# Kernel tuning notes

Measured on AMD Instinct MI355X. Metric: run time of the kernel, lower is better.

## Reference

```python
import jax, jax.numpy as jnp
import numpy as np

B, C, H, W = 64, 1280, 16, 16
S = H * W  # 256 spatial positions


def setup_inputs() -> dict:
    key = jax.random.key(0)
    kx, kk, kq, kv, kr, ka = jax.random.split(key, 6)
    x = jax.random.normal(kx, (B, C, H, W), dtype=jnp.float32)
    scale = 0.02
    Wk = jax.random.normal(kk, (C, C), dtype=jnp.float32) * scale
    Wq = jax.random.normal(kq, (C, C), dtype=jnp.float32) * scale
    Wv = jax.random.normal(kv, (C, C), dtype=jnp.float32) * scale
    Wr = jax.random.normal(kr, (C, C), dtype=jnp.float32) * scale
    # nn.Parameter(torch.zeros(1)) in the original; init nonzero so the
    # attention branch actually contributes.
    alpha = jax.random.normal(ka, (1,), dtype=jnp.float32) * 0.1
    return {"x": x, "Wk": Wk, "Wq": Wq, "Wv": Wv, "Wr": Wr, "alpha": alpha}


def reference(x, Wk, Wq, Wv, Wr, alpha):
    b, c = x.shape[0], x.shape[1]
    s = x.shape[2] * x.shape[3]
    xf = x.reshape(b, c, s)  # [B, C, S]
    # 1x1 convs == per-position channel matmuls
    K = jnp.einsum("oc,bcs->bos", Wk, xf)  # [B, C, S]
    Q = jnp.einsum("oc,bcs->bos", Wq, xf)
    V = jnp.einsum("oc,bcs->bos", Wv, xf)
    # scores[b,i,j] = sum_c K[b,c,i] * Q[b,c,j]
    scores = jnp.einsum("bci,bcj->bij", K, Q) / (c ** 0.5)  # [B, S, S]
    # torch.nn.Softmax2d on a 3D tensor applies softmax over dim=-3,
    # i.e. across the BATCH axis here (faithful to the original code).
    A = jax.nn.softmax(scores, axis=0)
    # attended[b,c,i] = sum_j A[b,i,j] * V[b,c,j]
    att = jnp.einsum("bij,bcj->bci", A, V)  # [B, C, S]
    refined = jnp.einsum("oc,bcs->bos", Wr, att).reshape(x.shape)
    out = alpha * refined + x  # use_alpha=True, skip connection
    return out
```

## Files before the change

kernel.cpp:

```cpp
#include <hip/hip_runtime.h>
#include <hip/hip_bf16.h>
#include <cstdint>
#include <cmath>

#define B_ 64
#define C_ 1280
#define S_ 256

typedef __attribute__((ext_vector_type(8))) short short8;
typedef __attribute__((ext_vector_type(4))) float f32x4;

typedef const __attribute__((address_space(1))) char gch;
typedef __attribute__((address_space(3))) char lch;

__device__ __forceinline__ void gload_lds16(const void* g, void* l) {
    __builtin_amdgcn_global_load_lds((gch*)g, (lch*)l, 16, 0, 0);
}

__device__ __forceinline__ unsigned short f2bu(float f) {
    __hip_bfloat16 h = __float2bfloat16(f);
    return *reinterpret_cast<unsigned short*>(&h);
}

__global__ void cvt_weights(const float* __restrict__ Wk, const float* __restrict__ Wq,
                            const float* __restrict__ Wv, const float* __restrict__ Wr,
                            __hip_bfloat16* __restrict__ Wcat, __hip_bfloat16* __restrict__ Wrb) {
    const int nW = C_ * C_;
    int i = blockIdx.x * blockDim.x + threadIdx.x;
    if (i >= 4 * nW) return;
    int seg = i / nW, off = i - seg * nW;
    float v;
    if (seg == 0) v = Wk[off];
    else if (seg == 1) v = Wq[off];
    else if (seg == 2) v = Wv[off];
    else v = Wr[off];
    if (seg < 3) Wcat[i] = __float2bfloat16(v);
    else Wrb[off] = __float2bfloat16(v);
}

__global__ void transpose_cvt(const float* __restrict__ x, __hip_bfloat16* __restrict__ xT) {
    __shared__ float tile[32][33];
    int b = blockIdx.z;
    int s0 = blockIdx.x * 32, c0 = blockIdx.y * 32;
    int tx = threadIdx.x, ty = threadIdx.y;
    const float* xb = x + (long)b * C_ * S_;
#pragma unroll
    for (int dy = 0; dy < 32; dy += 8)
        tile[ty + dy][tx] = xb[(long)(c0 + ty + dy) * S_ + s0 + tx];
    __syncthreads();
    __hip_bfloat16* xTb = xT + (long)b * S_ * C_;
#pragma unroll
    for (int dy = 0; dy < 32; dy += 8)
        xTb[(long)(s0 + ty + dy) * C_ + c0 + tx] = __float2bfloat16(tile[tx][ty + dy]);
}

__global__ void softmax_b(const float* __restrict__ scores, __hip_bfloat16* __restrict__ Abf) {
    int tid = blockIdx.x * blockDim.x + threadIdx.x;
    float r[64];
    float mx = -1e30f;
#pragma unroll
    for (int b = 0; b < 64; ++b) {
        r[b] = scores[(long)b * 65536 + tid];
        mx = fmaxf(mx, r[b]);
    }
    float sum = 0.f;
#pragma unroll
    for (int b = 0; b < 64; ++b) {
        r[b] = __expf(r[b] - mx);
        sum += r[b];
    }
    float inv = 1.0f / sum;
#pragma unroll
    for (int b = 0; b < 64; ++b)
        Abf[(long)b * 65536 + tid] = __float2bfloat16(r[b] * inv);
}


#define PH_TOP()                                                \
    do {                                                        \
        __builtin_amdgcn_sched_barrier(0);                      \
        __builtin_amdgcn_s_barrier();                           \
        asm volatile("s_waitcnt lgkmcnt(0)" ::: "memory");      \
        __builtin_amdgcn_sched_barrier(0);                      \
        __builtin_amdgcn_s_setprio(1);                          \
    } while (0)

#define PH_BOT()                                                \
    do {                                                        \
        __builtin_amdgcn_s_setprio(0);                          \
        __builtin_amdgcn_sched_barrier(0);                      \
        __builtin_amdgcn_s_barrier();                           \
    } while (0)

#define PH_BOT_WAIT(LAST_)                                          \
    do {                                                            \
        __builtin_amdgcn_s_setprio(0);                              \
        __builtin_amdgcn_sched_barrier(0);                          \
        if (LAST_) asm volatile("s_waitcnt vmcnt(0)" ::: "memory"); \
        else       asm volatile("s_waitcnt vmcnt(2)" ::: "memory"); \
        __builtin_amdgcn_s_barrier();                               \
    } while (0)

#define MFMA_Q(MO, NO, BFV)                                                                        \
    _Pragma("unroll") for (int m = 0; m < 4; ++m) {                                                \
        _Pragma("unroll") for (int n = 0; n < 2; ++n) {                                            \
            acc[m + MO][n + NO] = __builtin_amdgcn_mfma_f32_16x16x32_bf16(                         \
                af[m][0], BFV[n][0], acc[m + MO][n + NO], 0, 0, 0);                                \
            acc[m + MO][n + NO] = __builtin_amdgcn_mfma_f32_16x16x32_bf16(                         \
                af[m][1], BFV[n][1], acc[m + MO][n + NO], 0, 0, 0);                                \
        }                                                                                          \
    }

#define LOAD_A(SLOT, RO)                                  \
    _Pragma("unroll") for (int m = 0; m < 4; ++m) {       \
        af[m][0] = RD(SLOT, (RO) + m * 16 + l15, 0);      \
        af[m][1] = RD(SLOT, (RO) + m * 16 + l15, 1);      \
    }

#define LOAD_B(SLOT, BFV, NO)                                    \
    _Pragma("unroll") for (int n = 0; n < 2; ++n) {              \
        BFV[n][0] = RD(SLOT, rB0 + ((NO) + n) * 16 + l15, 0);    \
        BFV[n][1] = RD(SLOT, rB0 + ((NO) + n) * 16 + l15, 1);    \
    }

template <int MODE>
__global__ __launch_bounds__(512, 2) void gemm8p(
    const __hip_bfloat16* __restrict__ A, const __hip_bfloat16* __restrict__ Bm,
    __hip_bfloat16* __restrict__ Cc, int lda, int ldb, int ldc,
    int Kd, int tilesN, int nwg, int vTile,
    __hip_bfloat16* __restrict__ Vb,
    const float* __restrict__ xF, const float* __restrict__ alphaPtr,
    float* __restrict__ outF) {
    __shared__ char lds[131072];

    int bid = blockIdx.x;
    int cpx = nwg >> 3;
    int swz = (bid & 7) * cpx + (bid >> 3);
    int tm = swz / tilesN, tn = swz - tm * tilesN;

    int t = threadIdx.x;
    int lane = t & 63, w = t >> 6;
    int wm = w >> 2, wn = w & 3;
    int l15 = lane & 15, lhi = lane >> 4;
    int rB0 = (wn & 1) * 64;
    const int sA0 = wm, sB0 = 2 + (wn >> 1);
    const int sA1 = 4 + wm, sB1 = 6 + (wn >> 1);

    const __hip_bfloat16* aT = A + (long)tm * 256 * lda;
    const __hip_bfloat16* bT = Bm + (long)tn * 256 * ldb;

    int srow = t >> 3;
    int sc = ((t & 7) ^ (srow & 7)) * 8;
    const __hip_bfloat16* stA = aT + (long)srow * lda + sc;
    const __hip_bfloat16* stB = bT + (long)srow * ldb + sc;

    auto STAGE = [&](int kt, int j) {
        const __hip_bfloat16* p;
        long ldg;
        if (j < 2) { p = stA + (long)j * 128 * lda + kt * 64; ldg = lda; }
        else       { p = stB + (long)(j - 2) * 128 * ldb + kt * 64; ldg = ldb; }
        char* slot = lds + (((kt & 1) * 4 + j) << 14);
        gload_lds16(p, slot + t * 16);
        gload_lds16(p + 64 * ldg, slot + t * 16 + 8192);
    };

    auto RD = [&](int slotIdx, int row, int kk) -> short8 {
        const char* p = lds + (slotIdx << 14) + row * 128 +
                        ((((kk << 2) + lhi) ^ (row & 7)) << 4);
        return *reinterpret_cast<const short8*>(p);
    };

    f32x4 acc[8][4];
#pragma unroll
    for (int i = 0; i < 8; ++i)
#pragma unroll
        for (int j = 0; j < 4; ++j) acc[i][j] = (f32x4){0.f, 0.f, 0.f, 0.f};

    short8 af[4][2], b0v[2][2], b1v[2][2];

    STAGE(0, 0); STAGE(0, 1); STAGE(0, 2); STAGE(0, 3); STAGE(1, 0);
    asm volatile("s_waitcnt vmcnt(2)" ::: "memory");
    __builtin_amdgcn_s_barrier();
    __builtin_amdgcn_sched_barrier(0);

    const int NTH = Kd >> 7;
    for (int i = 0; i < NTH; ++i) {
        const bool last = (i == NTH - 1);
        const int kt0 = 2 * i, kt1 = 2 * i + 1;

        LOAD_A(sA0, 0)
        LOAD_B(sB0, b0v, 0)
        STAGE(kt1, 1);
        PH_TOP();
        MFMA_Q(0, 0, b0v)
        PH_BOT();

        LOAD_B(sB0, b1v, 2)
        STAGE(kt1, 2);
        PH_TOP();
        MFMA_Q(0, 2, b1v)
        PH_BOT();

        LOAD_A(sA0, 64)
        STAGE(kt1, 3);
        PH_TOP();
        MFMA_Q(4, 2, b1v)
        PH_BOT();

        if (!last) STAGE(kt0 + 2, 0);
        PH_TOP();
        MFMA_Q(4, 0, b0v)
        PH_BOT_WAIT(last);

        LOAD_A(sA1, 0)
        LOAD_B(sB1, b0v, 0)
        if (!last) STAGE(kt0 + 2, 1);
        PH_TOP();
        MFMA_Q(0, 0, b0v)
        PH_BOT();

        LOAD_B(sB1, b1v, 2)
        if (!last) STAGE(kt0 + 2, 2);
        PH_TOP();
        MFMA_Q(0, 2, b1v)
        PH_BOT();

        LOAD_A(sA1, 64)
        if (!last) STAGE(kt0 + 2, 3);
        PH_TOP();
        MFMA_Q(4, 2, b1v)
        PH_BOT();

        if (!last) STAGE(kt0 + 3, 0);
        PH_TOP();
        MFMA_Q(4, 0, b0v)
        __builtin_amdgcn_s_setprio(0);
        __builtin_amdgcn_sched_barrier(0);
        if (!last) asm volatile("s_waitcnt vmcnt(2)" ::: "memory");
        __builtin_amdgcn_s_barrier();
    }

    if constexpr (MODE == 1) {
        if (tn < vTile) {
            long crow0 = (long)tm * 256 + wm * 128;
            int cc0 = tn * 256 + wn * 64;
#pragma unroll
            for (int m = 0; m < 8; ++m) {
                long gm = crow0 + m * 16 + lhi * 4;
#pragma unroll
                for (int n = 0; n < 4; ++n) {
                    int gn = cc0 + n * 16 + l15;
#pragma unroll
                    for (int r = 0; r < 4; ++r)
                        Cc[(gm + r) * ldc + gn] = __float2bfloat16(acc[m][n][r]);
                }
            }
        } else {
            unsigned short* Vus = (unsigned short*)Vb;
            int cb0 = (tn - vTile) * 256 + wn * 64;
#pragma unroll
            for (int m = 0; m < 8; ++m) {
                int s0 = wm * 128 + m * 16 + lhi * 4;
#pragma unroll
                for (int n = 0; n < 4; ++n) {
                    int c = cb0 + n * 16 + l15;
                    ushort4 pk;
                    pk.x = f2bu(acc[m][n][0]);
                    pk.y = f2bu(acc[m][n][1]);
                    pk.z = f2bu(acc[m][n][2]);
                    pk.w = f2bu(acc[m][n][3]);
                    *reinterpret_cast<ushort4*>(&Vus[((long)(tm * 1280 + c) << 8) + s0]) = pk;
                }
            }
        }
    } else {
        float alpha = alphaPtr[0];
#pragma unroll
        for (int m = 0; m < 8; ++m) {
            int s0 = wm * 128 + m * 16 + lhi * 4;
#pragma unroll
            for (int n = 0; n < 4; ++n) {
                int c = tn * 256 + wn * 64 + n * 16 + l15;
                long base = ((long)(tm * 1280 + c) << 8) + s0;
                f32x4 xv = *reinterpret_cast<const f32x4*>(xF + base);
                f32x4 o;
#pragma unroll
                for (int r = 0; r < 4; ++r) o[r] = alpha * acc[m][n][r] + xv[r];
                *reinterpret_cast<f32x4*>(outF + base) = o;
            }
        }
    }
}

template <int MODE>
__global__ __launch_bounds__(256) void gemm_tn(
    const __hip_bfloat16* __restrict__ A, long aBatch, int lda,
    const __hip_bfloat16* __restrict__ Bm, long bBatch, int ldb,
    void* __restrict__ Cp, long cBatch, int ldc,
    int Kd, int tilesM, int tilesN, float scale) {
    __shared__ __hip_bfloat16 lA[128 * 32];
    __shared__ __hip_bfloat16 lB[128 * 32];

    int tiles = tilesM * tilesN;
    int blk = blockIdx.x;
    int b = blk / tiles;
    int rem = blk - b * tiles;
    int tm = rem / tilesN;
    int tn = rem - tm * tilesN;

    int t = threadIdx.x;
    int lane = t & 63;
    int w = t >> 6;
    int wm = w >> 1, wn = w & 1;
    int lane15 = lane & 15, lhi = lane >> 4;

    const __hip_bfloat16* Ab = A + (long)b * aBatch + (long)tm * 128 * lda;
    const __hip_bfloat16* Bb = Bm + (long)b * bBatch + (long)tn * 128 * ldb;

    f32x4 acc[4][4];
#pragma unroll
    for (int i = 0; i < 4; ++i)
#pragma unroll
        for (int j = 0; j < 4; ++j) acc[i][j] = (f32x4){0.f, 0.f, 0.f, 0.f};

    int e0 = t * 8;
    int r0 = e0 >> 5;
    int c0e = e0 & 31;

    for (int k0 = 0; k0 < Kd; k0 += 32) {
        gload_lds16(Ab + (long)r0 * lda + k0 + c0e, lA + e0);
        gload_lds16(Ab + (long)(r0 + 64) * lda + k0 + c0e, lA + 2048 + e0);
        gload_lds16(Bb + (long)r0 * ldb + k0 + c0e, lB + e0);
        gload_lds16(Bb + (long)(r0 + 64) * ldb + k0 + c0e, lB + 2048 + e0);
        __syncthreads();

        short8 af[4], bf[4];
#pragma unroll
        for (int i = 0; i < 4; ++i)
            af[i] = *reinterpret_cast<const short8*>(lA + (wm * 64 + i * 16 + lane15) * 32 + lhi * 8);
#pragma unroll
        for (int j = 0; j < 4; ++j)
            bf[j] = *reinterpret_cast<const short8*>(lB + (wn * 64 + j * 16 + lane15) * 32 + lhi * 8);
#pragma unroll
        for (int i = 0; i < 4; ++i)
#pragma unroll
            for (int j = 0; j < 4; ++j)
                acc[i][j] = __builtin_amdgcn_mfma_f32_16x16x32_bf16(af[i], bf[j], acc[i][j], 0, 0, 0);
        __syncthreads();
    }

    long cOff = (long)b * cBatch;
    if (MODE == 0) {
        __hip_bfloat16* Cb = (__hip_bfloat16*)Cp + cOff;
#pragma unroll
        for (int i = 0; i < 4; ++i) {
            int gm = tm * 128 + wm * 64 + i * 16 + lhi * 4;
#pragma unroll
            for (int j = 0; j < 4; ++j) {
                int gn = tn * 128 + wn * 64 + j * 16 + lane15;
#pragma unroll
                for (int r = 0; r < 4; ++r)
                    Cb[(long)(gm + r) * ldc + gn] = __float2bfloat16(acc[i][j][r]);
            }
        }
    } else {
        float* Cb = (float*)Cp + cOff;
#pragma unroll
        for (int i = 0; i < 4; ++i) {
            int gm = tm * 128 + wm * 64 + i * 16 + lhi * 4;
#pragma unroll
            for (int j = 0; j < 4; ++j) {
                int gn = tn * 128 + wn * 64 + j * 16 + lane15;
#pragma unroll
                for (int r = 0; r < 4; ++r)
                    Cb[(long)(gm + r) * ldc + gn] = acc[i][j][r] * scale;
            }
        }
    }
}

extern "C" void kernel_launch(void* const* d_in, const int* in_sizes, int n_in,
                              void* d_out, int out_size, void* d_ws, size_t ws_size,
                              hipStream_t stream) {
    const float* x = (const float*)d_in[0];
    const float* Wk = (const float*)d_in[1];
    const float* Wq = (const float*)d_in[2];
    const float* Wv = (const float*)d_in[3];
    const float* Wr = (const float*)d_in[4];
    const float* alphaPtr = (const float*)d_in[5];

    char* ws = (char*)d_ws;
    size_t off = 0;
    auto alloc = [&](size_t bytes) {
        char* p = ws + off;
        off += (bytes + 255) & ~(size_t)255;
        return p;
    };
    const size_t BSC = (size_t)B_ * S_ * C_;
    char* xTregion = alloc(BSC * 2);
    __hip_bfloat16* xT = (__hip_bfloat16*)xTregion;
    __hip_bfloat16* Wcat = (__hip_bfloat16*)alloc((size_t)3 * C_ * C_ * 2);
    __hip_bfloat16* Wrb = (__hip_bfloat16*)alloc((size_t)C_ * C_ * 2);
    __hip_bfloat16* KQ = (__hip_bfloat16*)alloc((size_t)B_ * S_ * 2 * C_ * 2);
    __hip_bfloat16* Abf = (__hip_bfloat16*)alloc((size_t)B_ * S_ * S_ * 2);
    __hip_bfloat16* Vb = (__hip_bfloat16*)alloc(BSC * 2);

    float* scores = (float*)xTregion;
    __hip_bfloat16* att_T = (__hip_bfloat16*)xTregion;

    const float scale = 1.0f / sqrtf((float)C_);
    int nW = C_ * C_;

    cvt_weights<<<(4 * nW + 255) / 256, 256, 0, stream>>>(Wk, Wq, Wv, Wr, Wcat, Wrb);

    transpose_cvt<<<dim3(S_ / 32, C_ / 32, B_), dim3(32, 8), 0, stream>>>(x, xT);

    gemm8p<1><<<960, 512, 0, stream>>>(xT, Wcat, KQ, C_, C_, 2 * C_,
                                       C_, 15, 960, 10, Vb, nullptr, nullptr, nullptr);

    gemm_tn<1><<<B_ * 4, 256, 0, stream>>>(KQ, (long)S_ * 2 * C_, 2 * C_,
                                           KQ + C_, (long)S_ * 2 * C_, 2 * C_,
                                           scores, (long)S_ * S_, S_,
                                           C_, 2, 2, scale);
    softmax_b<<<256, 256, 0, stream>>>(scores, Abf);

    gemm_tn<0><<<B_ * 20, 256, 0, stream>>>(Abf, (long)S_ * S_, S_,
                                            Vb, (long)C_ * S_, S_,
                                            att_T, (long)S_ * C_, C_,
                                            S_, 2, 10, 1.f);

    gemm8p<2><<<320, 512, 0, stream>>>(att_T, Wrb, nullptr, C_, C_, 0,
                                       C_, 5, 320, 0, nullptr, x, alphaPtr, (float*)d_out);
}
```

Before: 503.2 us.

## Precombine weight products to fold Q/K and V/R projections

Computes WqᵀWk (scaled) and Wr·Wv once per call as bf16 matrices. Scores then become G·xᵀ with G = x·(WqᵀWk), and the output becomes A applied to P = x·(WrWv)ᵀ. This removes one projection GEMM and the final refine GEMM, roughly halving the large-batch matmul work. In exchange it adds a C×C×C weight GEMM per call, extra intermediate buffers, and extra bf16 rounding of combined weights, which may affect accuracy.

```diff
diff --git a/kernel.cpp b/kernel.cpp
--- a/kernel.cpp
+++ b/kernel.cpp
@@ -22,20 +22,31 @@
     return *reinterpret_cast<unsigned short*>(&h);
 }
 
-__global__ void cvt_weights(const float* __restrict__ Wk, const float* __restrict__ Wq,
-                            const float* __restrict__ Wv, const float* __restrict__ Wr,
-                            __hip_bfloat16* __restrict__ Wcat, __hip_bfloat16* __restrict__ Wrb) {
-    const int nW = C_ * C_;
-    int i = blockIdx.x * blockDim.x + threadIdx.x;
-    if (i >= 4 * nW) return;
-    int seg = i / nW, off = i - seg * nW;
-    float v;
-    if (seg == 0) v = Wk[off];
-    else if (seg == 1) v = Wq[off];
-    else if (seg == 2) v = Wv[off];
-    else v = Wr[off];
-    if (seg < 3) Wcat[i] = __float2bfloat16(v);
-    else Wrb[off] = __float2bfloat16(v);
+__global__ void prep_weights(const float* __restrict__ Wk, const float* __restrict__ Wq,
+                             const float* __restrict__ Wv, const float* __restrict__ Wr,
+                             __hip_bfloat16* __restrict__ WqT, __hip_bfloat16* __restrict__ WkT,
+                             __hip_bfloat16* __restrict__ WvT, __hip_bfloat16* __restrict__ Wrb) {
+    __shared__ float tile[32][33];
+    int z = blockIdx.z;
+    const float* src = (z == 0) ? Wq : (z == 1) ? Wk : (z == 2) ? Wv : Wr;
+    __hip_bfloat16* dst = (z == 0) ? WqT : (z == 1) ? WkT : (z == 2) ? WvT : Wrb;
+    int r0 = blockIdx.x * 32, c0 = blockIdx.y * 32;
+    int tx = threadIdx.x, ty = threadIdx.y;
+    if (z == 3) {
+#pragma unroll
+        for (int dy = 0; dy < 32; dy += 8) {
+            int idx = (r0 + ty + dy) * C_ + c0 + tx;
+            dst[idx] = __float2bfloat16(src[idx]);
+        }
+        return;
+    }
+#pragma unroll
+    for (int dy = 0; dy < 32; dy += 8)
+        tile[ty + dy][tx] = src[(long)(r0 + ty + dy) * C_ + c0 + tx];
+    __syncthreads();
+#pragma unroll
+    for (int dy = 0; dy < 32; dy += 8)
+        dst[(long)(c0 + ty + dy) * C_ + r0 + tx] = __float2bfloat16(tile[tx][ty + dy]);
 }
 
 __global__ void transpose_cvt(const float* __restrict__ x, __hip_bfloat16* __restrict__ xT) {
@@ -123,14 +134,11 @@
         BFV[n][1] = RD(SLOT, rB0 + ((NO) + n) * 16 + l15, 1);    \
     }
 
-template <int MODE>
 __global__ __launch_bounds__(512, 2) void gemm8p(
     const __hip_bfloat16* __restrict__ A, const __hip_bfloat16* __restrict__ Bm,
     __hip_bfloat16* __restrict__ Cc, int lda, int ldb, int ldc,
     int Kd, int tilesN, int nwg, int vTile,
-    __hip_bfloat16* __restrict__ Vb,
-    const float* __restrict__ xF, const float* __restrict__ alphaPtr,
-    float* __restrict__ outF) {
+    __hip_bfloat16* __restrict__ Vb) {
     __shared__ char lds[131072];
 
     int bid = blockIdx.x;
@@ -240,53 +248,35 @@
         __builtin_amdgcn_s_barrier();
     }
 
-    if constexpr (MODE == 1) {
-        if (tn < vTile) {
-            long crow0 = (long)tm * 256 + wm * 128;
-            int cc0 = tn * 256 + wn * 64;
-#pragma unroll
-            for (int m = 0; m < 8; ++m) {
-                long gm = crow0 + m * 16 + lhi * 4;
-#pragma unroll
-                for (int n = 0; n < 4; ++n) {
-                    int gn = cc0 + n * 16 + l15;
-#pragma unroll
-                    for (int r = 0; r < 4; ++r)
-                        Cc[(gm + r) * ldc + gn] = __float2bfloat16(acc[m][n][r]);
-                }
-            }
-        } else {
-            unsigned short* Vus = (unsigned short*)Vb;
-            int cb0 = (tn - vTile) * 256 + wn * 64;
-#pragma unroll
-            for (int m = 0; m < 8; ++m) {
-                int s0 = wm * 128 + m * 16 + lhi * 4;
-#pragma unroll
-                for (int n = 0; n < 4; ++n) {
-                    int c = cb0 + n * 16 + l15;
-                    ushort4 pk;
-                    pk.x = f2bu(acc[m][n][0]);
-                    pk.y = f2bu(acc[m][n][1]);
-                    pk.z = f2bu(acc[m][n][2]);
-                    pk.w = f2bu(acc[m][n][3]);
-                    *reinterpret_cast<ushort4*>(&Vus[((long)(tm * 1280 + c) << 8) + s0]) = pk;
-                }
+    if (tn < vTile) {
+        long crow0 = (long)tm * 256 + wm * 128;
+        int cc0 = tn * 256 + wn * 64;
+#pragma unroll
+        for (int m = 0; m < 8; ++m) {
+            long gm = crow0 + m * 16 + lhi * 4;
+#pragma unroll
+            for (int n = 0; n < 4; ++n) {
+                int gn = cc0 + n * 16 + l15;
+#pragma unroll
+                for (int r = 0; r < 4; ++r)
+                    Cc[(gm + r) * ldc + gn] = __float2bfloat16(acc[m][n][r]);
             }
         }
     } else {
-        float alpha = alphaPtr[0];
+        unsigned short* Vus = (unsigned short*)Vb;
+        int cb0 = (tn - vTile) * 256 + wn * 64;
 #pragma unroll
         for (int m = 0; m < 8; ++m) {
             int s0 = wm * 128 + m * 16 + lhi * 4;
 #pragma unroll
             for (int n = 0; n < 4; ++n) {
-                int c = tn * 256 + wn * 64 + n * 16 + l15;
-                long base = ((long)(tm * 1280 + c) << 8) + s0;
-                f32x4 xv = *reinterpret_cast<const f32x4*>(xF + base);
-                f32x4 o;
-#pragma unroll
-                for (int r = 0; r < 4; ++r) o[r] = alpha * acc[m][n][r] + xv[r];
-                *reinterpret_cast<f32x4*>(outF + base) = o;
+                int c = cb0 + n * 16 + l15;
+                ushort4 pk;
+                pk.x = f2bu(acc[m][n][0]);
+                pk.y = f2bu(acc[m][n][1]);
+                pk.z = f2bu(acc[m][n][2]);
+                pk.w = f2bu(acc[m][n][3]);
+                *reinterpret_cast<ushort4*>(&Vus[((long)(tm * 1280 + c) << 8) + s0]) = pk;
             }
         }
     }
@@ -350,31 +340,158 @@
     }
 
     long cOff = (long)b * cBatch;
-    if (MODE == 0) {
-        __hip_bfloat16* Cb = (__hip_bfloat16*)Cp + cOff;
-#pragma unroll
-        for (int i = 0; i < 4; ++i) {
-            int gm = tm * 128 + wm * 64 + i * 16 + lhi * 4;
-#pragma unroll
-            for (int j = 0; j < 4; ++j) {
-                int gn = tn * 128 + wn * 64 + j * 16 + lane15;
-#pragma unroll
-                for (int r = 0; r < 4; ++r)
-                    Cb[(long)(gm + r) * ldc + gn] = __float2bfloat16(acc[i][j][r]);
-            }
+    float* Cb = (float*)Cp + cOff;
+#pragma unroll
+    for (int i = 0; i < 4; ++i) {
+        int gm = tm * 128 + wm * 64 + i * 16 + lhi * 4;
+#pragma unroll
+        for (int j = 0; j < 4; ++j) {
+            int gn = tn * 128 + wn * 64 + j * 16 + lane15;
+#pragma unroll
+            for (int r = 0; r < 4; ++r)
+                Cb[(long)(gm + r) * ldc + gn] = acc[i][j][r] * scale;
         }
-    } else {
-        float* Cb = (float*)Cp + cOff;
-#pragma unroll
-        for (int i = 0; i < 4; ++i) {
-            int gm = tm * 128 + wm * 64 + i * 16 + lhi * 4;
-#pragma unroll
-            for (int j = 0; j < 4; ++j) {
-                int gn = tn * 128 + wn * 64 + j * 16 + lane15;
-#pragma unroll
-                for (int r = 0; r < 4; ++r)
-                    Cb[(long)(gm + r) * ldc + gn] = acc[i][j][r] * scale;
-            }
+    }
+}
+
+__global__ __launch_bounds__(256) void gemm_weights(
+    const __hip_bfloat16* __restrict__ WqT, const __hip_bfloat16* __restrict__ WkT,
+    const __hip_bfloat16* __restrict__ Wrb, const __hip_bfloat16* __restrict__ WvT,
+    __hip_bfloat16* __restrict__ Bcat, float scale) {
+    __shared__ __hip_bfloat16 lA[128 * 32];
+    __shared__ __hip_bfloat16 lB[128 * 32];
+
+    int blk = blockIdx.x;
+    const __hip_bfloat16 *A, *Bm;
+    __hip_bfloat16* Cb;
+    float sc;
+    int rem;
+    if (blk < 100) { A = WqT; Bm = WkT; Cb = Bcat; sc = scale; rem = blk; }
+    else { A = Wrb; Bm = WvT; Cb = Bcat + 1280 * 1280; sc = 1.f; rem = blk - 100; }
+    int tm = rem / 10, tn = rem - tm * 10;
+
+    int t = threadIdx.x;
+    int lane = t & 63;
+    int w = t >> 6;
+    int wm = w >> 1, wn = w & 1;
+    int lane15 = lane & 15, lhi = lane >> 4;
+
+    const __hip_bfloat16* Ab = A + (long)tm * 128 * C_;
+    const __hip_bfloat16* Bb = Bm + (long)tn * 128 * C_;
+
+    f32x4 acc[4][4];
+#pragma unroll
+    for (int i = 0; i < 4; ++i)
+#pragma unroll
+        for (int j = 0; j < 4; ++j) acc[i][j] = (f32x4){0.f, 0.f, 0.f, 0.f};
+
+    int e0 = t * 8;
+    int r0 = e0 >> 5;
+    int c0e = e0 & 31;
+
+    for (int k0 = 0; k0 < C_; k0 += 32) {
+        gload_lds16(Ab + (long)r0 * C_ + k0 + c0e, lA + e0);
+        gload_lds16(Ab + (long)(r0 + 64) * C_ + k0 + c0e, lA + 2048 + e0);
+        gload_lds16(Bb + (long)r0 * C_ + k0 + c0e, lB + e0);
+        gload_lds16(Bb + (long)(r0 + 64) * C_ + k0 + c0e, lB + 2048 + e0);
+        __syncthreads();
+
+        short8 af[4], bf[4];
+#pragma unroll
+        for (int i = 0; i < 4; ++i)
+            af[i] = *reinterpret_cast<const short8*>(lA + (wm * 64 + i * 16 + lane15) * 32 + lhi * 8);
+#pragma unroll
+        for (int j = 0; j < 4; ++j)
+            bf[j] = *reinterpret_cast<const short8*>(lB + (wn * 64 + j * 16 + lane15) * 32 + lhi * 8);
+#pragma unroll
+        for (int i = 0; i < 4; ++i)
+#pragma unroll
+            for (int j = 0; j < 4; ++j)
+                acc[i][j] = __builtin_amdgcn_mfma_f32_16x16x32_bf16(af[i], bf[j], acc[i][j], 0, 0, 0);
+        __syncthreads();
+    }
+
+#pragma unroll
+    for (int i = 0; i < 4; ++i) {
+        int gm = tm * 128 + wm * 64 + i * 16 + lhi * 4;
+#pragma unroll
+        for (int j = 0; j < 4; ++j) {
+            int gn = tn * 128 + wn * 64 + j * 16 + lane15;
+#pragma unroll
+            for (int r = 0; r < 4; ++r)
+                Cb[(long)(gm + r) * C_ + gn] = __float2bfloat16(acc[i][j][r] * sc);
+        }
+    }
+}
+
+__global__ __launch_bounds__(256) void final_att(
+    const __hip_bfloat16* __restrict__ Abf, const __hip_bfloat16* __restrict__ P,
+    const float* __restrict__ x, const float* __restrict__ alphaPtr,
+    float* __restrict__ out) {
+    __shared__ __hip_bfloat16 lA[128 * 32];
+    __shared__ __hip_bfloat16 lB[128 * 32];
+
+    int blk = blockIdx.x;
+    int b = blk / 20;
+    int rem = blk - b * 20;
+    int tm = rem / 10, tn = rem - tm * 10;
+
+    int t = threadIdx.x;
+    int lane = t & 63;
+    int w = t >> 6;
+    int wm = w >> 1, wn = w & 1;
+    int lane15 = lane & 15, lhi = lane >> 4;
+
+    const __hip_bfloat16* Ab = Abf + (long)b * (S_ * S_) + (long)tm * 128 * S_;
+    const __hip_bfloat16* Bb = P + (long)b * (C_ * S_) + (long)tn * 128 * S_;
+
+    f32x4 acc[4][4];
+#pragma unroll
+    for (int i = 0; i < 4; ++i)
+#pragma unroll
+        for (int j = 0; j < 4; ++j) acc[i][j] = (f32x4){0.f, 0.f, 0.f, 0.f};
+
+    int e0 = t * 8;
+    int r0 = e0 >> 5;
+    int c0e = e0 & 31;
+
+#pragma unroll
+    for (int k0 = 0; k0 < S_; k0 += 32) {
+        gload_lds16(Ab + (long)r0 * S_ + k0 + c0e, lA + e0);
+        gload_lds16(Ab + (long)(r0 + 64) * S_ + k0 + c0e, lA + 2048 + e0);
+        gload_lds16(Bb + (long)r0 * S_ + k0 + c0e, lB + e0);
+        gload_lds16(Bb + (long)(r0 + 64) * S_ + k0 + c0e, lB + 2048 + e0);
+        __syncthreads();
+
+        short8 af[4], bf[4];
+#pragma unroll
+        for (int i = 0; i < 4; ++i)
+            af[i] = *reinterpret_cast<const short8*>(lA + (wm * 64 + i * 16 + lane15) * 32 + lhi * 8);
+#pragma unroll
+        for (int j = 0; j < 4; ++j)
+            bf[j] = *reinterpret_cast<const short8*>(lB + (wn * 64 + j * 16 + lane15) * 32 + lhi * 8);
+#pragma unroll
+        for (int i = 0; i < 4; ++i)
+#pragma unroll
+            for (int j = 0; j < 4; ++j)
+                acc[i][j] = __builtin_amdgcn_mfma_f32_16x16x32_bf16(af[i], bf[j], acc[i][j], 0, 0, 0);
+        __syncthreads();
+    }
+
+    float alpha = alphaPtr[0];
+    long bOff = (long)b * (C_ * S_);
+#pragma unroll
+    for (int i = 0; i < 4; ++i) {
+        int s0 = tm * 128 + wm * 64 + i * 16 + lhi * 4;
+#pragma unroll
+        for (int j = 0; j < 4; ++j) {
+            int c = tn * 128 + wn * 64 + j * 16 + lane15;
+            long base = bOff + (long)c * S_ + s0;
+            f32x4 xv = *reinterpret_cast<const f32x4*>(x + base);
+            f32x4 o;
+#pragma unroll
+            for (int r = 0; r < 4; ++r) o[r] = alpha * acc[i][j][r] + xv[r];
+            *reinterpret_cast<f32x4*>(out + base) = o;
         }
     }
 }
@@ -397,38 +514,34 @@
         return p;
     };
     const size_t BSC = (size_t)B_ * S_ * C_;
-    char* xTregion = alloc(BSC * 2);
-    __hip_bfloat16* xT = (__hip_bfloat16*)xTregion;
-    __hip_bfloat16* Wcat = (__hip_bfloat16*)alloc((size_t)3 * C_ * C_ * 2);
-    __hip_bfloat16* Wrb = (__hip_bfloat16*)alloc((size_t)C_ * C_ * 2);
-    __hip_bfloat16* KQ = (__hip_bfloat16*)alloc((size_t)B_ * S_ * 2 * C_ * 2);
+    const size_t CC = (size_t)C_ * C_;
+
+    __hip_bfloat16* xT = (__hip_bfloat16*)alloc(BSC * 2);
+    __hip_bfloat16* WqT = (__hip_bfloat16*)alloc(CC * 2);
+    __hip_bfloat16* WkT = (__hip_bfloat16*)alloc(CC * 2);
+    __hip_bfloat16* WvT = (__hip_bfloat16*)alloc(CC * 2);
+    __hip_bfloat16* Wrb = (__hip_bfloat16*)alloc(CC * 2);
+    __hip_bfloat16* Bcat = (__hip_bfloat16*)alloc(2 * CC * 2);
+    __hip_bfloat16* G = (__hip_bfloat16*)alloc(BSC * 2);
+    __hip_bfloat16* P = (__hip_bfloat16*)alloc(BSC * 2);
+    float* scores = (float*)alloc((size_t)B_ * S_ * S_ * 4);
     __hip_bfloat16* Abf = (__hip_bfloat16*)alloc((size_t)B_ * S_ * S_ * 2);
-    __hip_bfloat16* Vb = (__hip_bfloat16*)alloc(BSC * 2);
-
-    float* scores = (float*)xTregion;
-    __hip_bfloat16* att_T = (__hip_bfloat16*)xTregion;
 
     const float scale = 1.0f / sqrtf((float)C_);
-    int nW = C_ * C_;
-
-    cvt_weights<<<(4 * nW + 255) / 256, 256, 0, stream>>>(Wk, Wq, Wv, Wr, Wcat, Wrb);
+
+    prep_weights<<<dim3(40, 40, 4), dim3(32, 8), 0, stream>>>(Wk, Wq, Wv, Wr,
+                                                              WqT, WkT, WvT, Wrb);
+    gemm_weights<<<200, 256, 0, stream>>>(WqT, WkT, Wrb, WvT, Bcat, scale);
 
     transpose_cvt<<<dim3(S_ / 32, C_ / 32, B_), dim3(32, 8), 0, stream>>>(x, xT);
 
-    gemm8p<1><<<960, 512, 0, stream>>>(xT, Wcat, KQ, C_, C_, 2 * C_,
-                                       C_, 15, 960, 10, Vb, nullptr, nullptr, nullptr);
-
-    gemm_tn<1><<<B_ * 4, 256, 0, stream>>>(KQ, (long)S_ * 2 * C_, 2 * C_,
-                                           KQ + C_, (long)S_ * 2 * C_, 2 * C_,
+    gemm8p<<<640, 512, 0, stream>>>(xT, Bcat, G, C_, C_, C_, C_, 10, 640, 5, P);
+
+    gemm_tn<1><<<B_ * 4, 256, 0, stream>>>(G, (long)S_ * C_, C_,
+                                           xT, (long)S_ * C_, C_,
                                            scores, (long)S_ * S_, S_,
-                                           C_, 2, 2, scale);
+                                           C_, 2, 2, 1.0f);
     softmax_b<<<256, 256, 0, stream>>>(scores, Abf);
 
-    gemm_tn<0><<<B_ * 20, 256, 0, stream>>>(Abf, (long)S_ * S_, S_,
-                                            Vb, (long)C_ * S_, S_,
-                                            att_T, (long)S_ * C_, C_,
-                                            S_, 2, 10, 1.f);
-
-    gemm8p<2><<<320, 512, 0, stream>>>(att_T, Wrb, nullptr, C_, C_, 0,
-                                       C_, 5, 320, 0, nullptr, x, alphaPtr, (float*)d_out);
-}
+    final_att<<<1280, 256, 0, stream>>>(Abf, P, x, alphaPtr, (float*)d_out);
+}
```

Result: faster. 431.6 us (-14.2%).
